# Kernel tuning notes

Hardware: AMD Instinct MI355X
Metric: run time of the kernel (lower is better)

## Reference

```python
import jax, jax.numpy as jnp
import numpy as np

DIM = 384
HEADS = 8
SR = 2
EPS = 1e-5


def setup_inputs() -> dict:
    key = jax.random.key(0)
    ks = jax.random.split(key, 10)
    B, H, W, C = 16, 56, 56, DIM
    s = 0.02
    return {
        "x": jax.random.normal(ks[0], (B, H * W, C), jnp.float32),
        "qkv_w": jax.random.normal(ks[1], (3 * C, C), jnp.float32) * s,
        "qkv_b": jnp.zeros((3 * C,), jnp.float32),
        "proj_w": jax.random.normal(ks[2], (C, C), jnp.float32) * s,
        "proj_b": jnp.zeros((C,), jnp.float32),
        "lp_w": jax.random.normal(ks[3], (C, SR, SR), jnp.float32) * s,  # depthwise convT weight (C,1,sr,sr) squeezed
        "lp_b": jnp.zeros((C,), jnp.float32),
        "ln_w": jnp.ones((C,), jnp.float32),
        "ln_b": jnp.zeros((C,), jnp.float32),
        "H": 56,
        "W": 56,
    }


def reference(x, qkv_w, qkv_b, proj_w, proj_b, lp_w, lp_b, ln_w, ln_b, H, W):
    B, N, C = x.shape
    hd = C // HEADS
    scale = hd ** -0.5

    # AvgPool2d(kernel=(1,1), stride=(sr,sr)) == strided subsampling
    xi = x.transpose(0, 2, 1).reshape(B, C, H, W)[:, :, ::SR, ::SR]
    h, w = H // SR, W // SR
    n = h * w
    xs = xi.reshape(B, C, n).transpose(0, 2, 1)  # [B, n, C]

    qkv = (xs @ qkv_w.T + qkv_b).reshape(B, n, 3, HEADS, hd).transpose(2, 0, 3, 1, 4)
    q, k, v = qkv[0], qkv[1], qkv[2]  # each [B, heads, n, hd]

    attn = jax.nn.softmax(jnp.einsum('bhqd,bhkd->bhqk', q, k) * scale, axis=-1)
    o = jnp.einsum('bhqk,bhkd->bhqd', attn, v).transpose(0, 2, 1, 3).reshape(B, n, C)

    # ConvTranspose2d(C, C, kernel=sr, stride=sr, groups=C): each input pixel
    # expands to an sr x sr block scaled by the per-channel kernel.
    oi = o.transpose(0, 2, 1).reshape(B, C, h, w)
    up = jnp.einsum('bchw,cpq->bchpwq', oi, lp_w).reshape(B, C, H, W)
    up = up + lp_b[None, :, None, None]

    y = up.reshape(B, C, N).transpose(0, 2, 1)  # [B, N, C]
    mu = y.mean(-1, keepdims=True)
    var = y.var(-1, keepdims=True)
    y = (y - mu) * jax.lax.rsqrt(var + EPS) * ln_w + ln_b

    return y @ proj_w.T + proj_b
```

## Files before the change

### kernel.cpp

```cpp
#include <hip/hip_runtime.h>
#include <math.h>

#define CDIM 384
#define NHEADS 8
#define HD 48
#define NQ 784
#define NQPAD 832
#define NB 16
#define HWD 56
#define NPIX 3136
#define QK_SCALE (0.14433756729740643f * 1.4426950408889634f)
#define LN_EPS 1e-5f
#define WSCALE 16.0f
#define WUNSCALE 0.0625f

typedef _Float16 f16;
typedef _Float16 f16x4 __attribute__((ext_vector_type(4)));
typedef _Float16 f16x8 __attribute__((ext_vector_type(8)));
typedef float f32x4 __attribute__((ext_vector_type(4)));

__device__ __forceinline__ float waveSum(float v) {
#pragma unroll
  for (int o = 32; o > 0; o >>= 1) v += __shfl_xor(v, o);
  return v;
}

__device__ __forceinline__ float fast_exp2(float x) {
#if __has_builtin(__builtin_amdgcn_exp2f)
  return __builtin_amdgcn_exp2f(x);
#else
  return __expf(x * 0.6931471805599453f);
#endif
}

__device__ __forceinline__ void gload16(const void* g, void* l) {
  __builtin_amdgcn_global_load_lds(
      (const __attribute__((address_space(1))) void*)g,
      (__attribute__((address_space(3))) void*)l, 16, 0, 0);
}

__device__ __forceinline__ int xcd_chunk_lin(int b, int nwg) {
  const int c = b & 7, s = b >> 3;
  const int q = nwg >> 3, r = nwg & 7;
  const int off = (c < r) ? c * (q + 1) : r * (q + 1) + (c - r) * q;
  return off + s;
}

__global__ __launch_bounds__(256) void zero_kernel(float4* __restrict__ p,
                                                   int n4) {
  const int i = blockIdx.x * 256 + threadIdx.x;
  if (i < n4) p[i] = make_float4(0.f, 0.f, 0.f, 0.f);
}

__global__ __launch_bounds__(256) void pool_cast_kernel(
    const float* __restrict__ x, f16* __restrict__ xp) {
  const int i = (blockIdx.x * 256 + threadIdx.x) * 4;
  const int row = i / CDIM, col = i % CDIM;
  const int b = row / NQ, qi = row % NQ;
  const int hi = qi / 28, wi = qi % 28;
  const float4 v =
      *(const float4*)(x + ((size_t)(b * NPIX + hi * 112 + wi * 2)) * CDIM + col);
  f16x4 h;
  h.x = (f16)v.x; h.y = (f16)v.y; h.z = (f16)v.z; h.w = (f16)v.w;
  *(f16x4*)(xp + i) = h;
}

__global__ __launch_bounds__(256) void w_cast_kernel(
    const float* __restrict__ src, f16* __restrict__ dst, int n) {
  const int i = (blockIdx.x * 256 + threadIdx.x) * 4;
  if (i >= n) return;
  const float4 v = *(const float4*)(src + i);
  f16x4 h;
  h.x = (f16)v.x; h.y = (f16)v.y; h.z = (f16)v.z; h.w = (f16)v.w;
  *(f16x4*)(dst + i) = h;
}

__device__ __forceinline__ void mfma_tile_gemm_db(
    const f16* __restrict__ A, const f16* __restrict__ B, int m0, int n0,
    int K, f32x4 (&acc)[4][4], f16* As, f16* Bs) {
  const int t = threadIdx.x;
  const int lane = t & 63, w = t >> 6;
  const int wm = w >> 1, wn = w & 1;
  const int l15 = lane & 15, l4 = lane >> 4;
  const int rowS = t >> 2;
  const int kb = (t & 3) * 16;
  char* AsB = (char*)As;
  char* BsB = (char*)Bs;
  const char* Ag = (const char*)A + ((size_t)(m0 + rowS) * K) * 2 + kb;
  const char* Bg = (const char*)B + ((size_t)(n0 + rowS) * K) * 2 + kb;
  const size_t row64 = (size_t)64 * K * 2;

  gload16(Ag, AsB + t * 16);
  gload16(Ag + row64, AsB + 4096 + t * 16);
  gload16(Bg, BsB + t * 16);
  gload16(Bg + row64, BsB + 4096 + t * 16);

  int cur = 0;
  for (int k0 = 0; k0 < K; k0 += 32) {
    __syncthreads();
    if (k0 + 32 < K) {
      const int nb_ = cur ^ 1;
      const char* Ag2 = Ag + (size_t)(k0 + 32) * 2;
      const char* Bg2 = Bg + (size_t)(k0 + 32) * 2;
      gload16(Ag2, AsB + nb_ * 8192 + t * 16);
      gload16(Ag2 + row64, AsB + nb_ * 8192 + 4096 + t * 16);
      gload16(Bg2, BsB + nb_ * 8192 + t * 16);
      gload16(Bg2 + row64, BsB + nb_ * 8192 + 4096 + t * 16);
    }
    const char* Ab = AsB + cur * 8192;
    const char* Bb = BsB + cur * 8192;
    f16x8 af[4], bf[4];
#pragma unroll
    for (int i = 0; i < 4; ++i)
      af[i] = *(const f16x8*)(Ab + ((wm * 64 + i * 16 + l15) * 64 + l4 * 16));
#pragma unroll
    for (int j = 0; j < 4; ++j)
      bf[j] = *(const f16x8*)(Bb + ((wn * 64 + j * 16 + l15) * 64 + l4 * 16));
#pragma unroll
    for (int i = 0; i < 4; ++i)
#pragma unroll
      for (int j = 0; j < 4; ++j)
        acc[i][j] =
            __builtin_amdgcn_mfma_f32_16x16x32_f16(af[i], bf[j], acc[i][j], 0, 0, 0);
    cur ^= 1;
  }
}

__global__ __launch_bounds__(256) void qkv_mfma_kernel(
    const f16* __restrict__ xp, const f16* __restrict__ wh,
    const float* __restrict__ qkv_b, f16* __restrict__ qh,
    f16* __restrict__ kh, f16* __restrict__ vt) {
  __shared__ union SU {
    struct { f16 As[2 * 128 * 32]; f16 Bs[2 * 128 * 32]; } s;
    f16 Tr[128][136];
  } u;
  const int lin = xcd_chunk_lin(blockIdx.x, 882);
  const int m0 = (lin / 9) * 128, n0 = (lin % 9) * 128;
  f32x4 acc[4][4] = {};
  mfma_tile_gemm_db(xp, wh, m0, n0, CDIM, acc, u.s.As, u.s.Bs);

  const int t = threadIdx.x, lane = t & 63, w = t >> 6;
  const int wm = w >> 1, wn = w & 1;
  const int l15 = lane & 15, l4 = lane >> 4;
  const int sec = n0 / CDIM;
  const float scl = (sec == 0) ? QK_SCALE : 1.f;

  __syncthreads();

  if (sec < 2) {
#pragma unroll
    for (int j = 0; j < 4; ++j) {
      const int fl_ = wn * 64 + j * 16 + l15;
      const float bias = qkv_b[n0 + fl_];
#pragma unroll
      for (int i = 0; i < 4; ++i)
#pragma unroll
        for (int r = 0; r < 4; ++r)
          u.Tr[wm * 64 + i * 16 + l4 * 4 + r][fl_] =
              (f16)((acc[i][j][r] + bias) * scl);
    }
  } else {
#pragma unroll
    for (int j = 0; j < 4; ++j) {
      const int fl_ = wn * 64 + j * 16 + l15;
      const float bias = qkv_b[n0 + fl_];
#pragma unroll
      for (int i = 0; i < 4; ++i)
#pragma unroll
        for (int r = 0; r < 4; ++r)
          u.Tr[fl_][wm * 64 + i * 16 + l4 * 4 + r] = (f16)(acc[i][j][r] + bias);
    }
  }
  __syncthreads();

#pragma unroll
  for (int c = 0; c < 8; ++c) {
    const int v = c * 256 + t;
    const int rr = v >> 4, u16 = v & 15;
    if (sec < 2) {
      const int qi_l = rr, f_l = u16 * 8;
      const int fr = n0 + f_l - sec * CDIM;
      const int hh = fr / HD, d = fr - hh * HD;
      const int mm = m0 + qi_l, b = mm / NQ, tok = mm - b * NQ;
      f16* dst = (sec == 0 ? qh : kh) +
                 ((size_t)(b * NHEADS + hh) * NQ + tok) * HD + d;
      *(f16x8*)dst = *(const f16x8*)&u.Tr[qi_l][f_l];
    } else {
      const int f_l = rr, qi0 = u16 * 8;
      const int fr = n0 + f_l - 2 * CDIM;
      const int hh = fr / HD, d = fr - hh * HD;
      const int mm = m0 + qi0, b = mm / NQ, tok = mm - b * NQ;
      f16* dst = vt + ((size_t)(b * NHEADS + hh) * HD + d) * NQPAD + tok;
      *(f16x8*)dst = *(const f16x8*)&u.Tr[f_l][qi0];
    }
  }
}

__global__ __launch_bounds__(256) void flash_kernel(
    const f16* __restrict__ qh, const f16* __restrict__ kh,
    const f16* __restrict__ vt, f16* __restrict__ o16) {
  __shared__ f16 PQ[128 * 72];
  __shared__ f16 Ks[64][72];
  __shared__ f16 Vts[48][72];

  f16 (*Qs)[72] = (f16(*)[72])PQ;
  f16 (*Ps)[32][68] = (f16(*)[32][68])PQ;

  const int t = threadIdx.x;
  const int lane = t & 63, w = t >> 6;
  const int quad = lane >> 4, l15 = lane & 15;
  const int q0 = blockIdx.x * 128;
  const int bh = blockIdx.y;

  const f16* qg = qh + (size_t)bh * NQ * HD;
  const f16* kg = kh + (size_t)bh * NQ * HD;
  const f16* vg = vt + (size_t)bh * HD * NQPAD;

  {
    const f16x8 z8 = {};
    *(f16x8*)&Qs[t >> 1][48 + (t & 1) * 8] = z8;
    if (t < 128) *(f16x8*)&Ks[t >> 1][48 + (t & 1) * 8] = z8;
  }

#pragma unroll
  for (int c = 0; c < 3; ++c) {
    const int u = t + c * 256;
    const int row = u / 6, seg = u % 6;
    const int gr = min(q0 + row, NQ - 1);
    *(f16x8*)&Qs[row][seg * 8] =
        *(const f16x8*)(qg + (size_t)gr * HD + seg * 8);
  }
  __syncthreads();

  f16x8 qf0[2], qf1[2];
#pragma unroll
  for (int qa = 0; qa < 2; ++qa) {
    const int row = w * 32 + qa * 16 + l15;
    qf0[qa] = *(const f16x8*)&Qs[row][quad * 8];
    qf1[qa] = *(const f16x8*)&Qs[row][32 + quad * 8];
  }

  const f16* gp[3];
  f16* lp[3];
  int step[3];
#pragma unroll
  for (int c = 0; c < 3; ++c) {
    const int u = t + c * 256;
    if (u < 384) {
      const int row = u / 6, seg = u % 6;
      gp[c] = kg + (size_t)row * HD + seg * 8;
      lp[c] = &Ks[row][seg * 8];
      step[c] = 64 * HD;
    } else {
      const int uv = u - 384;
      const int row = uv >> 3, seg = uv & 7;
      gp[c] = vg + (size_t)row * NQPAD + seg * 8;
      lp[c] = &Vts[row][seg * 8];
      step[c] = 64;
    }
  }

  f16x8 rg[3];
#pragma unroll
  for (int c = 0; c < 3; ++c) {
    rg[c] = *(const f16x8*)gp[c];
    gp[c] += step[c];
  }

  f32x4 accO[2][3] = {};
  float l_[2][4] = {};

  for (int kt = 0; kt < 13; ++kt) {
#pragma unroll
    for (int c = 0; c < 3; ++c) *(f16x8*)lp[c] = rg[c];
    __syncthreads();
    if (kt < 12) {
#pragma unroll
      for (int c = 0; c < 3; ++c) {
        rg[c] = *(const f16x8*)gp[c];
        gp[c] += step[c];
      }
    }

    const bool last = (kt == 12);
#pragma unroll
    for (int j = 0; j < 4; ++j) {
      const f16x8 b0 = *(const f16x8*)&Ks[j * 16 + l15][quad * 8];
      const f16x8 b1 = *(const f16x8*)&Ks[j * 16 + l15][32 + quad * 8];
      f32x4 z0 = {}, z1 = {};
      z0 = __builtin_amdgcn_mfma_f32_16x16x32_f16(qf0[0], b0, z0, 0, 0, 0);
      const f32x4 sj0 = __builtin_amdgcn_mfma_f32_16x16x32_f16(qf1[0], b1, z0, 0, 0, 0);
      z1 = __builtin_amdgcn_mfma_f32_16x16x32_f16(qf0[1], b0, z1, 0, 0, 0);
      const f32x4 sj1 = __builtin_amdgcn_mfma_f32_16x16x32_f16(qf1[1], b1, z1, 0, 0, 0);
      const bool msk = last && (j >= 1);
#pragma unroll
      for (int r = 0; r < 4; ++r) {
        const float p0 = msk ? 0.f : fast_exp2(sj0[r]);
        const float p1 = msk ? 0.f : fast_exp2(sj1[r]);
        l_[0][r] += p0;
        l_[1][r] += p1;
        Ps[w][quad * 4 + r][j * 16 + l15] = (f16)p0;
        Ps[w][16 + quad * 4 + r][j * 16 + l15] = (f16)p1;
      }
    }

    f16x8 ap0[2], ap1[2];
#pragma unroll
    for (int qa = 0; qa < 2; ++qa) {
      const int row = qa * 16 + l15;
      const f16x4 a0 = *(const f16x4*)&Ps[w][row][quad * 8];
      const f16x4 a1 = *(const f16x4*)&Ps[w][row][quad * 8 + 4];
      const f16x4 a2 = *(const f16x4*)&Ps[w][row][32 + quad * 8];
      const f16x4 a3 = *(const f16x4*)&Ps[w][row][32 + quad * 8 + 4];
      ap0[qa] = __builtin_shufflevector(a0, a1, 0, 1, 2, 3, 4, 5, 6, 7);
      ap1[qa] = __builtin_shufflevector(a2, a3, 0, 1, 2, 3, 4, 5, 6, 7);
    }

#pragma unroll
    for (int jn = 0; jn < 3; ++jn) {
      const f16x8 v0 = *(const f16x8*)&Vts[jn * 16 + l15][quad * 8];
      const f16x8 v1 = *(const f16x8*)&Vts[jn * 16 + l15][32 + quad * 8];
#pragma unroll
      for (int qa = 0; qa < 2; ++qa) {
        accO[qa][jn] =
            __builtin_amdgcn_mfma_f32_16x16x32_f16(ap0[qa], v0, accO[qa][jn], 0, 0, 0);
        accO[qa][jn] =
            __builtin_amdgcn_mfma_f32_16x16x32_f16(ap1[qa], v1, accO[qa][jn], 0, 0, 0);
      }
    }
    __syncthreads();
  }

  const int b = bh >> 3, hh = bh & 7;
#pragma unroll
  for (int qa = 0; qa < 2; ++qa) {
#pragma unroll
    for (int r = 0; r < 4; ++r) {
      float rs = l_[qa][r];
      rs += __shfl_xor(rs, 1);
      rs += __shfl_xor(rs, 2);
      rs += __shfl_xor(rs, 4);
      rs += __shfl_xor(rs, 8);
      const int qrow = q0 + w * 32 + qa * 16 + quad * 4 + r;
      if (qrow < NQ) {
        const float inv = 1.f / rs;
#pragma unroll
        for (int jn = 0; jn < 3; ++jn)
          o16[((size_t)(b * NQ + qrow)) * CDIM + hh * HD + jn * 16 + l15] =
              (f16)(accO[qa][jn][r] * inv);
      }
    }
  }
}

__global__ __launch_bounds__(256) void stats_kernel(
    const f16* __restrict__ o16, const float* __restrict__ lp_w,
    const float* __restrict__ lp_b, float* __restrict__ stats) {
  const int m = blockIdx.x * 4 + (threadIdx.x >> 6);
  const int lane = threadIdx.x & 63;
  float s[4] = {}, ss[4] = {};
#pragma unroll
  for (int i = 0; i < 6; ++i) {
    const int c = lane + i * 64;
    const float ov = (float)o16[(size_t)m * CDIM + c];
    const float4 w4 = *(const float4*)(lp_w + c * 4);
    const float bb = lp_b[c];
    const float u0 = ov * w4.x + bb;
    const float u1 = ov * w4.y + bb;
    const float u2 = ov * w4.z + bb;
    const float u3 = ov * w4.w + bb;
    s[0] += u0; ss[0] += u0 * u0;
    s[1] += u1; ss[1] += u1 * u1;
    s[2] += u2; ss[2] += u2 * u2;
    s[3] += u3; ss[3] += u3 * u3;
  }
#pragma unroll
  for (int pq = 0; pq < 4; ++pq) {
    s[pq] = waveSum(s[pq]);
    ss[pq] = waveSum(ss[pq]);
  }
  if (lane < 4) {
    const float mu = s[lane] * (1.f / CDIM);
    const float var = ss[lane] * (1.f / CDIM) - mu * mu;
    stats[m * 8 + lane * 2] = mu;
    stats[m * 8 + lane * 2 + 1] = rsqrtf(var + LN_EPS);
  }
}

__global__ __launch_bounds__(256) void wprep_kernel(
    const float* __restrict__ pw, const float* __restrict__ lpw,
    const float* __restrict__ lnw, f16* __restrict__ wq) {
  const int i4 = (blockIdx.x * 256 + threadIdx.x) * 4;
  const int f = i4 / CDIM, c = i4 % CDIM;
  const int pq = f / CDIM, j = f % CDIM;
  const float4 wv = *(const float4*)(pw + (size_t)j * CDIM + c);
  const float4 ln = *(const float4*)(lnw + c);
  f16x4 h;
  h.x = (f16)(wv.x * lpw[(c + 0) * 4 + pq] * ln.x * WSCALE);
  h.y = (f16)(wv.y * lpw[(c + 1) * 4 + pq] * ln.y * WSCALE);
  h.z = (f16)(wv.z * lpw[(c + 2) * 4 + pq] * ln.z * WSCALE);
  h.w = (f16)(wv.w * lpw[(c + 3) * 4 + pq] * ln.w * WSCALE);
  *(f16x4*)(wq + i4) = h;
}

__global__ __launch_bounds__(64) void cvec_kernel(
    const float* __restrict__ pw, const float* __restrict__ lp_b,
    const float* __restrict__ ln_w, const float* __restrict__ ln_b,
    const float* __restrict__ pb, float* __restrict__ cvec) {
  const int j = blockIdx.x;
  const int lane = threadIdx.x;
  float a1 = 0.f, a2 = 0.f, a3 = 0.f;
#pragma unroll
  for (int i = 0; i < 6; ++i) {
    const int c = lane + i * 64;
    const float wv = pw[(size_t)j * CDIM + c];
    a1 += lp_b[c] * ln_w[c] * wv;
    a2 += ln_w[c] * wv;
    a3 += ln_b[c] * wv;
  }
  a1 = waveSum(a1);
  a2 = waveSum(a2);
  a3 = waveSum(a3);
  if (lane == 0) {
    cvec[j] = a1;
    cvec[CDIM + j] = a2;
    cvec[2 * CDIM + j] = a3 + pb[j];
  }
}

__global__ __launch_bounds__(256) void projfused_kernel(
    const f16* __restrict__ o16, const f16* __restrict__ wq,
    const float* __restrict__ stats, const float* __restrict__ cvec,
    float* __restrict__ out) {
  __shared__ f16 As[2 * 128 * 32];
  __shared__ f16 Bs[2 * 128 * 32];
  const int lin = xcd_chunk_lin(blockIdx.x, 1176);
  const int m0 = (lin / 12) * 128, n0 = (lin % 12) * 128;
  f32x4 acc[4][4] = {};
  mfma_tile_gemm_db(o16, wq, m0, n0, CDIM, acc, As, Bs);

  const int t = threadIdx.x, lane = t & 63, w = t >> 6;
  const int wm = w >> 1, wn = w & 1;
  const int l15 = lane & 15, l4 = lane >> 4;
  const int pq = n0 / CDIM;
  const int p = pq >> 1, q = pq & 1;
  const int c0 = n0 - pq * CDIM;

  float C1[4], C2[4], C3[4];
#pragma unroll
  for (int j = 0; j < 4; ++j) {
    const int col = c0 + wn * 64 + j * 16 + l15;
    C1[j] = cvec[col];
    C2[j] = cvec[CDIM + col];
    C3[j] = cvec[2 * CDIM + col];
  }

#pragma unroll
  for (int i = 0; i < 4; ++i) {
#pragma unroll
    for (int r = 0; r < 4; ++r) {
      const int m = m0 + wm * 64 + i * 16 + l4 * 4 + r;
      const int b = m / NQ, n = m % NQ;
      const int hi2 = n / 28, wi2 = n % 28;
      const float mu = stats[m * 8 + pq * 2];
      const float rstd = stats[m * 8 + pq * 2 + 1];
      const int pix = (hi2 * 2 + p) * HWD + (wi2 * 2 + q);
      float* orow = out + ((size_t)(b * NPIX + pix)) * CDIM;
#pragma unroll
      for (int j = 0; j < 4; ++j) {
        const int col = c0 + wn * 64 + j * 16 + l15;
        orow[col] = rstd * (acc[i][j][r] * WUNSCALE + C1[j] - mu * C2[j]) + C3[j];
      }
    }
  }
}

extern "C" void kernel_launch(void* const* d_in, const int* in_sizes, int n_in,
                              void* d_out, int out_size, void* d_ws,
                              size_t ws_size, hipStream_t stream) {
  const float* x      = (const float*)d_in[0];
  const float* qkv_w  = (const float*)d_in[1];
  const float* qkv_b  = (const float*)d_in[2];
  const float* proj_w = (const float*)d_in[3];
  const float* proj_b = (const float*)d_in[4];
  const float* lp_w   = (const float*)d_in[5];
  const float* lp_b   = (const float*)d_in[6];
  const float* ln_w   = (const float*)d_in[7];
  const float* ln_b   = (const float*)d_in[8];
  float* out = (float*)d_out;

  float* ws = (float*)d_ws;
  f16* o16 = (f16*)ws;
  float* zreg = ws + 2408448;
  f16* qh = (f16*)zreg;
  f16* kh = qh + (size_t)128 * NQ * HD;
  f16* vt = kh + (size_t)128 * NQ * HD;
  float* rest = zreg + 7372800;
  f16* xp = (f16*)rest;
  f16* qkv_wh = xp + (size_t)12544 * CDIM;
  float* rest2 = rest + 2408448 + 221184;
  f16* wq = (f16*)rest2;
  float* cvec = rest2 + 1179648;
  float* stats = cvec + 1152;

  zero_kernel<<<dim3(2496), 256, 0, stream>>>((float4*)(zreg + 4816896), 638976);

  pool_cast_kernel<<<dim3(4704), 256, 0, stream>>>(x, xp);
  w_cast_kernel<<<dim3(432), 256, 0, stream>>>(qkv_w, qkv_wh, 1152 * CDIM);
  qkv_mfma_kernel<<<dim3(882), 256, 0, stream>>>(xp, qkv_wh, qkv_b, qh, kh, vt);

  flash_kernel<<<dim3(7, 128), 256, 0, stream>>>(qh, kh, vt, o16);

  stats_kernel<<<dim3(3136), 256, 0, stream>>>(o16, lp_w, lp_b, stats);
  wprep_kernel<<<dim3(576), 256, 0, stream>>>(proj_w, lp_w, ln_w, wq);
  cvec_kernel<<<dim3(384), 64, 0, stream>>>(proj_w, lp_b, ln_w, ln_b, proj_b,
                                            cvec);

  projfused_kernel<<<dim3(1176), 256, 0, stream>>>(o16, wq, stats, cvec, out);
}
```

Measured before the change: 254.6 us.

## Merge prep kernels into one launch, zero only V padding, swizzle flash LDS

Five small prep kernels (pool-cast, weight cast, proj weight prep, bias vector, and zeroing) become a single block-indexed kernel. This cuts launch overhead and inter-kernel gaps. The full zeroing of the V region is replaced by zeroing only the padded tail columns of each vt row. Separately, the flash kernel's K and V shared tiles drop their row padding and use an XOR swizzle on 16-byte segments to avoid bank conflicts. The narrower zeroing relies on the qkv kernel writing every non-pad entry.

After: 242.8 us. 4.7% less time.

```diff
diff --git a/kernel.cpp b/kernel.cpp
--- a/kernel.cpp
+++ b/kernel.cpp
@@ -46,33 +46,69 @@
   return off + s;
 }
 
-__global__ __launch_bounds__(256) void zero_kernel(float4* __restrict__ p,
-                                                   int n4) {
-  const int i = blockIdx.x * 256 + threadIdx.x;
-  if (i < n4) p[i] = make_float4(0.f, 0.f, 0.f, 0.f);
-}
-
-__global__ __launch_bounds__(256) void pool_cast_kernel(
-    const float* __restrict__ x, f16* __restrict__ xp) {
-  const int i = (blockIdx.x * 256 + threadIdx.x) * 4;
-  const int row = i / CDIM, col = i % CDIM;
-  const int b = row / NQ, qi = row % NQ;
-  const int hi = qi / 28, wi = qi % 28;
-  const float4 v =
-      *(const float4*)(x + ((size_t)(b * NPIX + hi * 112 + wi * 2)) * CDIM + col);
-  f16x4 h;
-  h.x = (f16)v.x; h.y = (f16)v.y; h.z = (f16)v.z; h.w = (f16)v.w;
-  *(f16x4*)(xp + i) = h;
-}
-
-__global__ __launch_bounds__(256) void w_cast_kernel(
-    const float* __restrict__ src, f16* __restrict__ dst, int n) {
-  const int i = (blockIdx.x * 256 + threadIdx.x) * 4;
-  if (i >= n) return;
-  const float4 v = *(const float4*)(src + i);
-  f16x4 h;
-  h.x = (f16)v.x; h.y = (f16)v.y; h.z = (f16)v.z; h.w = (f16)v.w;
-  *(f16x4*)(dst + i) = h;
+__global__ __launch_bounds__(256) void prep_kernel(
+    const float* __restrict__ x, f16* __restrict__ xp,
+    const float* __restrict__ qkv_w, f16* __restrict__ qkv_wh,
+    f16* __restrict__ vt, const float* __restrict__ pw,
+    const float* __restrict__ lpw, const float* __restrict__ lnw,
+    const float* __restrict__ lp_b, const float* __restrict__ ln_b,
+    const float* __restrict__ pb, f16* __restrict__ wq,
+    float* __restrict__ cvec) {
+  const int blk = blockIdx.x, t = threadIdx.x;
+  if (blk < 4704) {
+    const int i = (blk * 256 + t) * 4;
+    const int row = i / CDIM, col = i % CDIM;
+    const int b = row / NQ, qi = row % NQ;
+    const int hi = qi / 28, wi = qi % 28;
+    const float4 v =
+        *(const float4*)(x + ((size_t)(b * NPIX + hi * 112 + wi * 2)) * CDIM + col);
+    f16x4 h;
+    h.x = (f16)v.x; h.y = (f16)v.y; h.z = (f16)v.z; h.w = (f16)v.w;
+    *(f16x4*)(xp + i) = h;
+  } else if (blk < 5136) {
+    const int i = ((blk - 4704) * 256 + t) * 4;
+    const float4 v = *(const float4*)(qkv_w + i);
+    f16x4 h;
+    h.x = (f16)v.x; h.y = (f16)v.y; h.z = (f16)v.z; h.w = (f16)v.w;
+    *(f16x4*)(qkv_wh + i) = h;
+  } else if (blk < 5280) {
+    const int idx = (blk - 5136) * 256 + t;
+    const int row = idx / 6, off = idx % 6;
+    float4* p = (float4*)vt + (size_t)row * 104 + 98 + off;
+    *p = make_float4(0.f, 0.f, 0.f, 0.f);
+  } else if (blk < 5856) {
+    const int i4 = ((blk - 5280) * 256 + t) * 4;
+    const int f = i4 / CDIM, c = i4 % CDIM;
+    const int pq = f / CDIM, j = f % CDIM;
+    const float4 wv = *(const float4*)(pw + (size_t)j * CDIM + c);
+    const float4 ln = *(const float4*)(lnw + c);
+    f16x4 h;
+    h.x = (f16)(wv.x * lpw[(c + 0) * 4 + pq] * ln.x * WSCALE);
+    h.y = (f16)(wv.y * lpw[(c + 1) * 4 + pq] * ln.y * WSCALE);
+    h.z = (f16)(wv.z * lpw[(c + 2) * 4 + pq] * ln.z * WSCALE);
+    h.w = (f16)(wv.w * lpw[(c + 3) * 4 + pq] * ln.w * WSCALE);
+    *(f16x4*)(wq + i4) = h;
+  } else {
+    const int j = (blk - 5856) * 4 + (t >> 6);
+    const int lane = t & 63;
+    float a1 = 0.f, a2 = 0.f, a3 = 0.f;
+#pragma unroll
+    for (int i = 0; i < 6; ++i) {
+      const int c = lane + i * 64;
+      const float wv = pw[(size_t)j * CDIM + c];
+      a1 += lp_b[c] * lnw[c] * wv;
+      a2 += lnw[c] * wv;
+      a3 += ln_b[c] * wv;
+    }
+    a1 = waveSum(a1);
+    a2 = waveSum(a2);
+    a3 = waveSum(a3);
+    if (lane == 0) {
+      cvec[j] = a1;
+      cvec[CDIM + j] = a2;
+      cvec[2 * CDIM + j] = a3 + pb[j];
+    }
+  }
 }
 
 __device__ __forceinline__ void mfma_tile_gemm_db(
@@ -200,8 +236,8 @@
     const f16* __restrict__ qh, const f16* __restrict__ kh,
     const f16* __restrict__ vt, f16* __restrict__ o16) {
   __shared__ f16 PQ[128 * 72];
-  __shared__ f16 Ks[64][72];
-  __shared__ f16 Vts[48][72];
+  __shared__ f16 Ks[64][64];
+  __shared__ f16 Vts[48][64];
 
   f16 (*Qs)[72] = (f16(*)[72])PQ;
   f16 (*Ps)[32][68] = (f16(*)[32][68])PQ;
@@ -219,7 +255,10 @@
   {
     const f16x8 z8 = {};
     *(f16x8*)&Qs[t >> 1][48 + (t & 1) * 8] = z8;
-    if (t < 128) *(f16x8*)&Ks[t >> 1][48 + (t & 1) * 8] = z8;
+    if (t < 128) {
+      const int row = t >> 1, zc = 6 + (t & 1);
+      *(f16x8*)&Ks[row][(zc ^ (row & 7)) * 8] = z8;
+    }
   }
 
 #pragma unroll
@@ -249,13 +288,13 @@
     if (u < 384) {
       const int row = u / 6, seg = u % 6;
       gp[c] = kg + (size_t)row * HD + seg * 8;
-      lp[c] = &Ks[row][seg * 8];
+      lp[c] = &Ks[row][(seg ^ (row & 7)) * 8];
       step[c] = 64 * HD;
     } else {
       const int uv = u - 384;
       const int row = uv >> 3, seg = uv & 7;
       gp[c] = vg + (size_t)row * NQPAD + seg * 8;
-      lp[c] = &Vts[row][seg * 8];
+      lp[c] = &Vts[row][(seg ^ (row & 7)) * 8];
       step[c] = 64;
     }
   }
@@ -285,8 +324,9 @@
     const bool last = (kt == 12);
 #pragma unroll
     for (int j = 0; j < 4; ++j) {
-      const f16x8 b0 = *(const f16x8*)&Ks[j * 16 + l15][quad * 8];
-      const f16x8 b1 = *(const f16x8*)&Ks[j * 16 + l15][32 + quad * 8];
+      const int krow = j * 16 + l15, ksw = krow & 7;
+      const f16x8 b0 = *(const f16x8*)&Ks[krow][(quad ^ ksw) * 8];
+      const f16x8 b1 = *(const f16x8*)&Ks[krow][((4 + quad) ^ ksw) * 8];
       f32x4 z0 = {}, z1 = {};
       z0 = __builtin_amdgcn_mfma_f32_16x16x32_f16(qf0[0], b0, z0, 0, 0, 0);
       const f32x4 sj0 = __builtin_amdgcn_mfma_f32_16x16x32_f16(qf1[0], b1, z0, 0, 0, 0);
@@ -318,8 +358,9 @@
 
 #pragma unroll
     for (int jn = 0; jn < 3; ++jn) {
-      const f16x8 v0 = *(const f16x8*)&Vts[jn * 16 + l15][quad * 8];
-      const f16x8 v1 = *(const f16x8*)&Vts[jn * 16 + l15][32 + quad * 8];
+      const int vrow = jn * 16 + l15, vsw = vrow & 7;
+      const f16x8 v0 = *(const f16x8*)&Vts[vrow][(quad ^ vsw) * 8];
+      const f16x8 v1 = *(const f16x8*)&Vts[vrow][((4 + quad) ^ vsw) * 8];
 #pragma unroll
       for (int qa = 0; qa < 2; ++qa) {
         accO[qa][jn] =
@@ -387,47 +428,6 @@
   }
 }
 
-__global__ __launch_bounds__(256) void wprep_kernel(
-    const float* __restrict__ pw, const float* __restrict__ lpw,
-    const float* __restrict__ lnw, f16* __restrict__ wq) {
-  const int i4 = (blockIdx.x * 256 + threadIdx.x) * 4;
-  const int f = i4 / CDIM, c = i4 % CDIM;
-  const int pq = f / CDIM, j = f % CDIM;
-  const float4 wv = *(const float4*)(pw + (size_t)j * CDIM + c);
-  const float4 ln = *(const float4*)(lnw + c);
-  f16x4 h;
-  h.x = (f16)(wv.x * lpw[(c + 0) * 4 + pq] * ln.x * WSCALE);
-  h.y = (f16)(wv.y * lpw[(c + 1) * 4 + pq] * ln.y * WSCALE);
-  h.z = (f16)(wv.z * lpw[(c + 2) * 4 + pq] * ln.z * WSCALE);
-  h.w = (f16)(wv.w * lpw[(c + 3) * 4 + pq] * ln.w * WSCALE);
-  *(f16x4*)(wq + i4) = h;
-}
-
-__global__ __launch_bounds__(64) void cvec_kernel(
-    const float* __restrict__ pw, const float* __restrict__ lp_b,
-    const float* __restrict__ ln_w, const float* __restrict__ ln_b,
-    const float* __restrict__ pb, float* __restrict__ cvec) {
-  const int j = blockIdx.x;
-  const int lane = threadIdx.x;
-  float a1 = 0.f, a2 = 0.f, a3 = 0.f;
-#pragma unroll
-  for (int i = 0; i < 6; ++i) {
-    const int c = lane + i * 64;
-    const float wv = pw[(size_t)j * CDIM + c];
-    a1 += lp_b[c] * ln_w[c] * wv;
-    a2 += ln_w[c] * wv;
-    a3 += ln_b[c] * wv;
-  }
-  a1 = waveSum(a1);
-  a2 = waveSum(a2);
-  a3 = waveSum(a3);
-  if (lane == 0) {
-    cvec[j] = a1;
-    cvec[CDIM + j] = a2;
-    cvec[2 * CDIM + j] = a3 + pb[j];
-  }
-}
-
 __global__ __launch_bounds__(256) void projfused_kernel(
     const f16* __restrict__ o16, const f16* __restrict__ wq,
     const float* __restrict__ stats, const float* __restrict__ cvec,
@@ -503,18 +503,15 @@
   float* cvec = rest2 + 1179648;
   float* stats = cvec + 1152;
 
-  zero_kernel<<<dim3(2496), 256, 0, stream>>>((float4*)(zreg + 4816896), 638976);
-
-  pool_cast_kernel<<<dim3(4704), 256, 0, stream>>>(x, xp);
-  w_cast_kernel<<<dim3(432), 256, 0, stream>>>(qkv_w, qkv_wh, 1152 * CDIM);
+  prep_kernel<<<dim3(5952), 256, 0, stream>>>(x, xp, qkv_w, qkv_wh, vt, proj_w,
+                                              lp_w, ln_w, lp_b, ln_b, proj_b,
+                                              wq, cvec);
+
   qkv_mfma_kernel<<<dim3(882), 256, 0, stream>>>(xp, qkv_wh, qkv_b, qh, kh, vt);
 
   flash_kernel<<<dim3(7, 128), 256, 0, stream>>>(qh, kh, vt, o16);
 
   stats_kernel<<<dim3(3136), 256, 0, stream>>>(o16, lp_w, lp_b, stats);
-  wprep_kernel<<<dim3(576), 256, 0, stream>>>(proj_w, lp_w, ln_w, wq);
-  cvec_kernel<<<dim3(384), 64, 0, stream>>>(proj_w, lp_b, ln_w, ln_b, proj_b,
-                                            cvec);
 
   projfused_kernel<<<dim3(1176), 256, 0, stream>>>(o16, wq, stats, cvec, out);
 }
```
